# Optimization experiments

Hardware: AMD Instinct MI355X
Metric: run time of the kernel (lower is better)

## Reference

```python
import jax, jax.numpy as jnp
import numpy as np
import math

B, S, D, H, WIDTH, NHW = 8, 1024, 512, 8, 8, 2
DK = D // H
S2 = S + 2 * WIDTH


def setup_inputs() -> dict:
    key = jax.random.key(0)
    ks = jax.random.split(key, 12)
    sc = 1.0 / math.sqrt(D)
    return {
        "x": jax.random.normal(ks[0], (B, S, D), jnp.float32),
        "l_attn_W": jax.random.normal(ks[1], (4, D, D), jnp.float32) * sc,  # q,k,v,out
        "l_attn_b": jnp.zeros((4, D), jnp.float32),
        "r_attn_W": jax.random.normal(ks[2], (4, D, D), jnp.float32) * sc,
        "r_attn_b": jnp.zeros((4, D), jnp.float32),
        "left_pad": jax.random.normal(ks[3], (WIDTH, D), jnp.float32) * sc,
        "right_pad": jax.random.normal(ks[4], (WIDTH, D), jnp.float32) * sc,
        "left_w": jax.random.normal(ks[5], (WIDTH + 1,), jnp.float32),
        "right_w": jax.random.normal(ks[6], (WIDTH + 1,), jnp.float32),
        "l_hw_W": jax.random.normal(ks[7], (NHW, D, 2 * D), jnp.float32) * sc,
        "l_hw_b": jnp.zeros((NHW, 2 * D), jnp.float32),
        "r_hw_W": jax.random.normal(ks[8], (NHW, D, 2 * D), jnp.float32) * sc,
        "r_hw_b": jnp.zeros((NHW, 2 * D), jnp.float32),
    }


def _mha(x, W, b, mask):
    # x: [B, S2, D]; W: [4, D, D]; mask: [1, S2, S2] bool (True = keep)
    q = (x @ W[0] + b[0]).reshape(B, S2, H, DK)
    k = (x @ W[1] + b[1]).reshape(B, S2, H, DK)
    v = (x @ W[2] + b[2]).reshape(B, S2, H, DK)
    scores = jnp.einsum('bihd,bjhd->bhij', q, k) / math.sqrt(DK)
    scores = jnp.where(mask[:, None], scores, jnp.float32(-1e9))
    p = jax.nn.softmax(scores, axis=-1)
    o = jnp.einsum('bhij,bjhd->bihd', p, v).reshape(B, S2, D)
    return o @ W[3] + b[3]


def _highway(x, Ws, bs):
    # AllenNLP-style Highway: projected -> [nonlinear | gate]
    for i in range(NHW):
        proj = x @ Ws[i] + bs[i]
        nl = jax.nn.relu(proj[..., :D])
        g = jax.nn.sigmoid(proj[..., D:])
        x = g * x + (1.0 - g) * nl
    return x


def reference(x, l_attn_W, l_attn_b, r_attn_W, r_attn_b, left_pad, right_pad,
              left_w, right_w, l_hw_W, l_hw_b, r_hw_W, r_hw_b):
    new_in = jnp.concatenate([
        jnp.broadcast_to(left_pad, (B, WIDTH, D)), x,
        jnp.broadcast_to(right_pad, (B, WIDTH, D))], axis=1)  # [B, S2, D]
    idx = jnp.arange(S2)
    diff = idx[:, None] - idx[None, :]
    lmask = ((diff >= 0) & (diff <= WIDTH + 1))[None]          # attend to [i-width-1, i]
    rmask = ((diff <= 0) & (diff >= -(WIDTH + 1)))[None]       # attend to [i, i+width+1]
    nl_attn = _mha(new_in, l_attn_W, l_attn_b, lmask)
    nr_attn = _mha(new_in, r_attn_W, r_attn_b, rmask)
    left_out = nl_attn[:, WIDTH:WIDTH + S, :]   # position end = start + width
    right_out = nr_attn[:, WIDTH:WIDTH + S, :]
    # relative-position weighted sliding windows (vectorized over all steps)
    lrel = sum(left_w[j] * new_in[:, j:j + S, :] for j in range(WIDTH + 1))
    rrel = sum(right_w[j] * new_in[:, WIDTH + j:WIDTH + j + S, :] for j in range(WIDTH + 1))
    left_out = _highway(left_out + lrel, l_hw_W, l_hw_b)
    right_out = _highway(right_out + rrel, r_hw_W, r_hw_b)
    out = jnp.concatenate([left_out, right_out], axis=-1)  # [B, S, 2D]
    return out[None]  # [1, B, S, 2D] matching torch stack layout
```

## Files before the change

### kernel.cpp

```cpp
#include <hip/hip_runtime.h>


#define B_ 8
#define S_ 1024
#define D_ 512
#define H_ 8
#define DK_ 64
#define WIDTH_ 8
#define S2_ 1040
#define NHW_ 2

typedef short bf16x8 __attribute__((ext_vector_type(8)));
typedef float f32x4 __attribute__((ext_vector_type(4)));

__device__ __forceinline__ float us2f(unsigned short u) {
  union { unsigned int i; float f; } c; c.i = ((unsigned int)u) << 16; return c.f;
}
__device__ __forceinline__ unsigned short f2us(float f) {
  union { float f; unsigned int i; } c; c.f = f;
  unsigned int x = c.i;
  return (unsigned short)((x + 0x7fffu + ((x >> 16) & 1u)) >> 16);
}
__device__ __forceinline__ unsigned int pack2(float a, float b) {
  return (unsigned int)f2us(a) | ((unsigned int)f2us(b) << 16);
}
__device__ __forceinline__ void async16(const void* g, void* l) {
  __builtin_amdgcn_global_load_lds(
      (const __attribute__((address_space(1))) void*)g,
      (__attribute__((address_space(3))) void*)l, 16, 0, 0);
}
__device__ __forceinline__ void unpack8(uint4 u, float* f) {
  unsigned int w[4] = {u.x, u.y, u.z, u.w};
  #pragma unroll
  for (int c = 0; c < 4; ++c) {
    union { unsigned int i; float g; } lo, hi;
    lo.i = w[c] << 16;
    hi.i = w[c] & 0xffff0000u;
    f[2 * c] = lo.g;
    f[2 * c + 1] = hi.g;
  }
}

__global__ __launch_bounds__(256) void k_prep(
    const float* __restrict__ x,
    const float* __restrict__ lpad, const float* __restrict__ rpad,
    const float* __restrict__ lW, const float* __restrict__ rW,
    const float* __restrict__ lb, const float* __restrict__ rb,
    const float* __restrict__ lhwW, const float* __restrict__ rhwW,
    unsigned short* __restrict__ WTall, unsigned short* __restrict__ WTp,
    unsigned short* __restrict__ hWT,
    unsigned short* __restrict__ nin, float* __restrict__ qkvbias)
{
  __shared__ float tile[32][33];
  const size_t DD = (size_t)D_ * D_;
  int bx = blockIdx.x;
  int tx = threadIdx.x & 31, ty = threadIdx.x >> 5;

  if (bx < 2048) {
    int sl = bx >> 8, rem = bx & 255;
    int side = sl >> 2, slice = sl & 3;
    int c0 = (rem & 15) * 32, r0 = (rem >> 4) * 32;
    const float* src = (side ? rW : lW) + (size_t)slice * DD;
    unsigned short* dst = (slice < 3) ? WTall + (size_t)(side * 3 + slice) * DD
                                      : WTp + (size_t)side * DD;
    #pragma unroll
    for (int i = 0; i < 4; ++i)
      tile[ty + i * 8][tx] = src[(size_t)(r0 + ty + i * 8) * D_ + c0 + tx];
    __syncthreads();
    #pragma unroll
    for (int i = 0; i < 4; ++i)
      dst[(size_t)(c0 + ty + i * 8) * D_ + r0 + tx] = f2us(tile[tx][ty + i * 8]);
    return;
  }
  if (bx < 4096) {
    int idx = bx - 2048;
    int sl = idx >> 9, rem = idx & 511;
    int c0 = (rem & 31) * 32, r0 = (rem >> 5) * 32;
    const float* src = ((sl >> 1) ? rhwW : lhwW) + (size_t)(sl & 1) * 512 * 1024;
    unsigned short* dst = hWT + (size_t)sl * 1024 * 512;
    #pragma unroll
    for (int i = 0; i < 4; ++i)
      tile[ty + i * 8][tx] = src[(size_t)(r0 + ty + i * 8) * 1024 + c0 + tx];
    __syncthreads();
    #pragma unroll
    for (int i = 0; i < 4; ++i) {
      int c = c0 + ty + i * 8;
      int q = (2 * ((c & 511) >> 4) + (c >= 512 ? 1 : 0)) * 16 + (c & 15);
      dst[(size_t)q * 512 + r0 + tx] = f2us(tile[tx][ty + i * 8]);
    }
    return;
  }
  int gid = (bx - 4096) * 256 + threadIdx.x;
  const int NTH = B_ * S2_ * 64;
  if (gid >= NTH) {
    int t = gid - NTH;
    if (t < 1536) qkvbias[t] = lb[t];
    else if (t < 3072) qkvbias[t] = rb[t - 1536];
    return;
  }
  int c8 = (gid & 63) << 3;
  int row = gid >> 6;
  int b = row / S2_;
  int t = row - b * S2_;
  const float* src;
  if (t < WIDTH_)            src = lpad + (size_t)t * D_ + c8;
  else if (t >= S_ + WIDTH_) src = rpad + (size_t)(t - S_ - WIDTH_) * D_ + c8;
  else                       src = x + ((size_t)b * S_ + (t - WIDTH_)) * D_ + c8;
  float4 a = *reinterpret_cast<const float4*>(src);
  float4 c = *reinterpret_cast<const float4*>(src + 4);
  uint4 o;
  o.x = pack2(a.x, a.y); o.y = pack2(a.z, a.w);
  o.z = pack2(c.x, c.y); o.w = pack2(c.z, c.w);
  *reinterpret_cast<uint4*>(nin + (size_t)row * D_ + c8) = o;
}

__global__ __launch_bounds__(256) void k_gemm_mfma(
    const unsigned short* __restrict__ A,
    const unsigned short* __restrict__ BT,
    const float* __restrict__ bias,
    unsigned short* __restrict__ C,
    int M, int N, int K)
{
  __shared__ unsigned short As[128 * 64];
  __shared__ unsigned short Bs[128 * 64];

  const int tid = threadIdx.x;
  const int w = tid >> 6;
  const int l = tid & 63;
  const int bm = blockIdx.y * 128;
  const int bn = blockIdx.x * 128;
  const int wrow = (w >> 1) * 64;
  const int wcol = (w & 1) * 64;

  const int lr = l >> 3;
  const int sk = (((l & 7) ^ lr) & 7) * 8;
  const unsigned short* Ap = A + (size_t)(bm + w * 8 + lr) * K + sk;
  const unsigned short* Bp = BT + (size_t)(bn + w * 8 + lr) * K + sk;
  unsigned short* lA = &As[w * 512];
  unsigned short* lB = &Bs[w * 512];
  const size_t K32 = (size_t)32 * K;

  const int fl = l & 15;
  const int fq = l >> 4;
  const int fx = fl & 7;

  f32x4 acc[4][4];
  #pragma unroll
  for (int mi = 0; mi < 4; ++mi)
    #pragma unroll
    for (int ni = 0; ni < 4; ++ni) acc[mi][ni] = (f32x4){0.f, 0.f, 0.f, 0.f};

  for (int k0 = 0; k0 < K; k0 += 64) {
    #pragma unroll
    for (int r = 0; r < 4; ++r) {
      async16(Ap + k0 + r * K32, lA + r * 2048);
      async16(Bp + k0 + r * K32, lB + r * 2048);
    }
    __syncthreads();
    #pragma unroll
    for (int s = 0; s < 2; ++s) {
      bf16x8 af[4], bfr[4];
      #pragma unroll
      for (int mi = 0; mi < 4; ++mi)
        af[mi] = *reinterpret_cast<const bf16x8*>(
            &As[(wrow + mi * 16 + fl) * 64 + (((s * 4 + fq) ^ fx) * 8)]);
      #pragma unroll
      for (int ni = 0; ni < 4; ++ni)
        bfr[ni] = *reinterpret_cast<const bf16x8*>(
            &Bs[(wcol + ni * 16 + fl) * 64 + (((s * 4 + fq) ^ fx) * 8)]);
      #pragma unroll
      for (int mi = 0; mi < 4; ++mi)
        #pragma unroll
        for (int ni = 0; ni < 4; ++ni)
          acc[mi][ni] = __builtin_amdgcn_mfma_f32_16x16x32_bf16(
              af[mi], bfr[ni], acc[mi][ni], 0, 0, 0);
    }
    __syncthreads();
  }

  float bv[4];
  #pragma unroll
  for (int ni = 0; ni < 4; ++ni) bv[ni] = bias[bn + wcol + ni * 16 + fl];

  const int rbase = (l >> 4) * 4;
  #pragma unroll
  for (int mi = 0; mi < 4; ++mi) {
    #pragma unroll
    for (int r = 0; r < 4; ++r) {
      int row = bm + wrow + mi * 16 + rbase + r;
      unsigned short* Cp = C + (size_t)row * N + bn + wcol + fl;
      #pragma unroll
      for (int ni = 0; ni < 4; ++ni)
        Cp[ni * 16] = f2us(acc[mi][ni][r] + bv[ni]);
    }
  }
}

__global__ __launch_bounds__(256) void k_gemm_proj(
    const unsigned short* __restrict__ ctx,
    const unsigned short* __restrict__ WTp,
    const unsigned short* __restrict__ nin,
    const float* __restrict__ lb3, const float* __restrict__ rb3,
    const float* __restrict__ wrel0, const float* __restrict__ wrel1,
    unsigned short* __restrict__ hwx)
{
  __shared__ unsigned short smem[128 * 136];
  unsigned short* As = smem;
  unsigned short* Bs = smem + 8192;
  const int K = 512, N = 512;
  const size_t MS = (size_t)B_ * S_ * D_;

  const int z = blockIdx.z;
  const unsigned short* A = ctx + (size_t)z * MS;
  const unsigned short* BT = WTp + (size_t)z * 512 * 512;
  const float* bias = z ? rb3 : lb3;
  const float* wrel = z ? wrel1 : wrel0;
  const int off = z * WIDTH_;

  const int tid = threadIdx.x;
  const int w = tid >> 6;
  const int l = tid & 63;
  const int bm = blockIdx.y * 128;
  const int bn = blockIdx.x * 128;
  const int wrow = (w >> 1) * 64;
  const int wcol = (w & 1) * 64;

  const int lr = l >> 3;
  const int sk = (((l & 7) ^ lr) & 7) * 8;
  const unsigned short* Ap = A + (size_t)(bm + w * 8 + lr) * K + sk;
  const unsigned short* Bp = BT + (size_t)(bn + w * 8 + lr) * K + sk;
  unsigned short* lA = &As[w * 512];
  unsigned short* lB = &Bs[w * 512];
  const size_t K32 = (size_t)32 * K;

  const int fl = l & 15;
  const int fq = l >> 4;
  const int fx = fl & 7;

  f32x4 acc[4][4];
  #pragma unroll
  for (int mi = 0; mi < 4; ++mi)
    #pragma unroll
    for (int ni = 0; ni < 4; ++ni) acc[mi][ni] = (f32x4){0.f, 0.f, 0.f, 0.f};

  for (int k0 = 0; k0 < K; k0 += 64) {
    #pragma unroll
    for (int r = 0; r < 4; ++r) {
      async16(Ap + k0 + r * K32, lA + r * 2048);
      async16(Bp + k0 + r * K32, lB + r * 2048);
    }
    __syncthreads();
    #pragma unroll
    for (int s = 0; s < 2; ++s) {
      bf16x8 af[4], bfr[4];
      #pragma unroll
      for (int mi = 0; mi < 4; ++mi)
        af[mi] = *reinterpret_cast<const bf16x8*>(
            &As[(wrow + mi * 16 + fl) * 64 + (((s * 4 + fq) ^ fx) * 8)]);
      #pragma unroll
      for (int ni = 0; ni < 4; ++ni)
        bfr[ni] = *reinterpret_cast<const bf16x8*>(
            &Bs[(wcol + ni * 16 + fl) * 64 + (((s * 4 + fq) ^ fx) * 8)]);
      #pragma unroll
      for (int mi = 0; mi < 4; ++mi)
        #pragma unroll
        for (int ni = 0; ni < 4; ++ni)
          acc[mi][ni] = __builtin_amdgcn_mfma_f32_16x16x32_bf16(
              af[mi], bfr[ni], acc[mi][ni], 0, 0, 0);
    }
    __syncthreads();
  }

  float bv[4];
  #pragma unroll
  for (int ni = 0; ni < 4; ++ni) bv[ni] = bias[bn + wcol + ni * 16 + fl];
  const int rbase = (l >> 4) * 4;
  #pragma unroll
  for (int mi = 0; mi < 4; ++mi)
    #pragma unroll
    for (int r = 0; r < 4; ++r)
      #pragma unroll
      for (int ni = 0; ni < 4; ++ni)
        smem[(wrow + mi * 16 + rbase + r) * 136 + wcol + ni * 16 + fl] =
            f2us(acc[mi][ni][r] + bv[ni]);
  __syncthreads();

  const int trow = tid >> 4;
  const int tcol = (tid & 15) * 8;
  const float w0 = wrel[0], w1 = wrel[1], w2 = wrel[2], w3 = wrel[3],
              w4 = wrel[4], w5 = wrel[5], w6 = wrel[6], w7 = wrel[7],
              w8 = wrel[8];
  const float wj[9] = {w0, w1, w2, w3, w4, w5, w6, w7, w8};
  #pragma unroll
  for (int i = 0; i < 8; ++i) {
    int r = trow + i * 16;
    int gr = bm + r;
    int b = gr >> 10, s = gr & (S_ - 1);
    float a8[8];
    unpack8(*reinterpret_cast<const uint4*>(&smem[r * 136 + tcol]), a8);
    const unsigned short* np =
        nin + ((size_t)b * S2_ + off + s) * D_ + bn + tcol;
    #pragma unroll
    for (int j = 0; j < 9; ++j) {
      float nf[8];
      unpack8(*reinterpret_cast<const uint4*>(np + (size_t)j * D_), nf);
      #pragma unroll
      for (int e = 0; e < 8; ++e) a8[e] += wj[j] * nf[e];
    }
    uint4 o;
    o.x = pack2(a8[0], a8[1]); o.y = pack2(a8[2], a8[3]);
    o.z = pack2(a8[4], a8[5]); o.w = pack2(a8[6], a8[7]);
    *reinterpret_cast<uint4*>(
        hwx + (size_t)z * MS + (size_t)gr * D_ + bn + tcol) = o;
  }
}

template <bool FINAL>
__global__ __launch_bounds__(256) void k_gemm_hw(
    const unsigned short* __restrict__ Xsrc,
    const unsigned short* __restrict__ BT, size_t bStrZ,
    const float* __restrict__ bias0, const float* __restrict__ bias1,
    unsigned short* __restrict__ Obf,
    float* __restrict__ Ofp)
{
  __shared__ unsigned short As[128 * 64];
  __shared__ unsigned short Bs[128 * 64];
  const int K = 512;
  const size_t MS = (size_t)B_ * S_ * D_;

  const int z = blockIdx.z;
  const unsigned short* A = Xsrc + (size_t)z * MS;
  BT += (size_t)z * bStrZ;
  const float* bias = z ? bias1 : bias0;

  const int tid = threadIdx.x;
  const int w = tid >> 6;
  const int l = tid & 63;
  const int bm = blockIdx.y * 128;
  const int bn = blockIdx.x * 128;
  const int wrow = (w >> 1) * 64;
  const int wcol = (w & 1) * 64;

  const int lr = l >> 3;
  const int sk = (((l & 7) ^ lr) & 7) * 8;
  const unsigned short* Ap = A + (size_t)(bm + w * 8 + lr) * K + sk;
  const unsigned short* Bp = BT + (size_t)(bn + w * 8 + lr) * K + sk;
  unsigned short* lA = &As[w * 512];
  unsigned short* lB = &Bs[w * 512];
  const size_t K32 = (size_t)32 * K;

  const int fl = l & 15;
  const int fq = l >> 4;
  const int fx = fl & 7;

  f32x4 acc[4][4];
  #pragma unroll
  for (int mi = 0; mi < 4; ++mi)
    #pragma unroll
    for (int ni = 0; ni < 4; ++ni) acc[mi][ni] = (f32x4){0.f, 0.f, 0.f, 0.f};

  for (int k0 = 0; k0 < K; k0 += 64) {
    #pragma unroll
    for (int r = 0; r < 4; ++r) {
      async16(Ap + k0 + r * K32, lA + r * 2048);
      async16(Bp + k0 + r * K32, lB + r * 2048);
    }
    __syncthreads();
    #pragma unroll
    for (int s = 0; s < 2; ++s) {
      bf16x8 af[4], bfr[4];
      #pragma unroll
      for (int mi = 0; mi < 4; ++mi)
        af[mi] = *reinterpret_cast<const bf16x8*>(
            &As[(wrow + mi * 16 + fl) * 64 + (((s * 4 + fq) ^ fx) * 8)]);
      #pragma unroll
      for (int ni = 0; ni < 4; ++ni)
        bfr[ni] = *reinterpret_cast<const bf16x8*>(
            &Bs[(wcol + ni * 16 + fl) * 64 + (((s * 4 + fq) ^ fx) * 8)]);
      #pragma unroll
      for (int mi = 0; mi < 4; ++mi)
        #pragma unroll
        for (int ni = 0; ni < 4; ++ni)
          acc[mi][ni] = __builtin_amdgcn_mfma_f32_16x16x32_bf16(
              af[mi], bfr[ni], acc[mi][ni], 0, 0, 0);
    }
    __syncthreads();
  }

  const int ocb = ((bn + wcol) >> 1) + fl;
  float bnl[2], bg[2];
  #pragma unroll
  for (int p = 0; p < 2; ++p) {
    bnl[p] = bias[ocb + p * 16];
    bg[p]  = bias[512 + ocb + p * 16];
  }

  const int rbase = (l >> 4) * 4;
  #pragma unroll
  for (int mi = 0; mi < 4; ++mi) {
    #pragma unroll
    for (int r = 0; r < 4; ++r) {
      int row = bm + wrow + mi * 16 + rbase + r;
      #pragma unroll
      for (int p = 0; p < 2; ++p) {
        int oc = ocb + p * 16;
        float nl = fmaxf(acc[mi][2 * p][r] + bnl[p], 0.f);
        float g  = 1.f / (1.f + __expf(-(acc[mi][2 * p + 1][r] + bg[p])));
        float xv = us2f(A[(size_t)row * 512 + oc]);
        float res = g * xv + (1.f - g) * nl;
        if (FINAL) Ofp[(size_t)row * 1024 + z * 512 + oc] = res;
        else       Obf[(size_t)z * MS + (size_t)row * 512 + oc] = f2us(res);
      }
    }
  }
}

__global__ __launch_bounds__(256) void k_attn_window(
    const unsigned short* __restrict__ qkv,
    unsigned short* __restrict__ ctx)
{
  int wid = (blockIdx.x * 256 + threadIdx.x) >> 6;
  int lane = threadIdx.x & 63;
  int s = wid & (S_ - 1);
  int b = (wid >> 10) & (B_ - 1);
  int dir = wid >> 13;
  int i = s + WIDTH_;

  const size_t base = (size_t)b * S2_ * 3072 + dir * 1536;
  const int c0 = lane * 8;

  float qf[8];
  unpack8(*reinterpret_cast<const uint4*>(qkv + base + (size_t)i * 3072 + c0), qf);

  float sc[10];
  float mx = -1e30f;
  #pragma unroll
  for (int t = 0; t < 10; ++t) {
    int j = (dir == 0) ? (i - 9 + t) : (i + t);
    float sv = -1e30f;
    if (j >= 0 && j < S2_) {
      float kf[8];
      unpack8(*reinterpret_cast<const uint4*>(
          qkv + base + (size_t)j * 3072 + 512 + c0), kf);
      float p = qf[0] * kf[0];
      #pragma unroll
      for (int e = 1; e < 8; ++e) p += qf[e] * kf[e];
      p += __shfl_xor(p, 1);
      p += __shfl_xor(p, 2);
      p += __shfl_xor(p, 4);
      sv = p * 0.125f;
    }
    sc[t] = sv;
    mx = fmaxf(mx, sv);
  }

  float denom = 0.f;
  #pragma unroll
  for (int t = 0; t < 10; ++t) {
    sc[t] = (sc[t] > -1e29f) ? __expf(sc[t] - mx) : 0.f;
    denom += sc[t];
  }
  float inv = 1.f / denom;

  float acc[8] = {0.f, 0.f, 0.f, 0.f, 0.f, 0.f, 0.f, 0.f};
  #pragma unroll
  for (int t = 0; t < 10; ++t) {
    int j = (dir == 0) ? (i - 9 + t) : (i + t);
    if (j >= 0 && j < S2_) {
      float vf[8];
      unpack8(*reinterpret_cast<const uint4*>(
          qkv + base + (size_t)j * 3072 + 1024 + c0), vf);
      float p = sc[t];
      #pragma unroll
      for (int e = 0; e < 8; ++e) acc[e] += p * vf[e];
    }
  }

  uint4 o;
  o.x = pack2(acc[0] * inv, acc[1] * inv);
  o.y = pack2(acc[2] * inv, acc[3] * inv);
  o.z = pack2(acc[4] * inv, acc[5] * inv);
  o.w = pack2(acc[6] * inv, acc[7] * inv);
  *reinterpret_cast<uint4*>(
      ctx + (((size_t)dir * B_ + b) * S_ + s) * D_ + c0) = o;
}

extern "C" void kernel_launch(void* const* d_in, const int* in_sizes, int n_in,
                              void* d_out, int out_size, void* d_ws, size_t ws_size,
                              hipStream_t stream) {
  const float* x    = (const float*)d_in[0];
  const float* lW   = (const float*)d_in[1];
  const float* lb   = (const float*)d_in[2];
  const float* rW   = (const float*)d_in[3];
  const float* rb   = (const float*)d_in[4];
  const float* lpad = (const float*)d_in[5];
  const float* rpad = (const float*)d_in[6];
  const float* lw   = (const float*)d_in[7];
  const float* rw   = (const float*)d_in[8];
  const float* lhwW = (const float*)d_in[9];
  const float* lhwb = (const float*)d_in[10];
  const float* rhwW = (const float*)d_in[11];
  const float* rhwb = (const float*)d_in[12];
  float* out = (float*)d_out;
  unsigned short* ws = (unsigned short*)d_ws;

  const size_t NIN  = (size_t)B_ * S2_ * D_;
  const size_t NQKV = (size_t)B_ * S2_ * 3072;
  const size_t MS   = (size_t)B_ * S_ * D_;
  const size_t DD   = (size_t)D_ * D_;
  const size_t LHW  = (size_t)1024 * 512;

  unsigned short* nin   = ws;
  unsigned short* qkv   = nin + NIN;
  unsigned short* ctx   = qkv + NQKV;
  unsigned short* hwx   = ctx + 2 * MS;
  unsigned short* hwy   = hwx + 2 * MS;
  unsigned short* WTall = hwy + 2 * MS;
  unsigned short* WTp   = WTall + 6 * DD;
  unsigned short* hWT   = WTp + 2 * DD;
  float* qkvbias        = (float*)(hWT + 4 * LHW);

  k_prep<<<6188, 256, 0, stream>>>(x, lpad, rpad, lW, rW, lb, rb, lhwW, rhwW,
                                   WTall, WTp, hWT, nin, qkvbias);

  const int MQ = B_ * S2_;

  {
    dim3 g(3072 / 128, MQ / 128, 1);
    k_gemm_mfma<<<g, 256, 0, stream>>>(nin, WTall, qkvbias, qkv, MQ, 3072, D_);
  }

  k_attn_window<<<(2 * B_ * S_) / 4, 256, 0, stream>>>(qkv, ctx);

  {
    dim3 g(D_ / 128, (B_ * S_) / 128, 2);
    k_gemm_proj<<<g, 256, 0, stream>>>(ctx, WTp, nin, lb + 3 * D_, rb + 3 * D_,
                                       lw, rw, hwx);
  }

  {
    dim3 g(1024 / 128, (B_ * S_) / 128, 2);
    k_gemm_hw<false><<<g, 256, 0, stream>>>(hwx, hWT, 2 * LHW,
                                            lhwb, rhwb, hwy, nullptr);
    k_gemm_hw<true><<<g, 256, 0, stream>>>(hwy, hWT + LHW, 2 * LHW,
                                           lhwb + 1024, rhwb + 1024,
                                           nullptr, out);
  }
}
```

Baseline: 249.1 us.

## Replace 128x128 GEMMs with double-buffered 256x256 eight-wave MFMA kernel

Replaces the QKV and highway GEMM kernels with a single templated 256x256-tile kernel that uses 512 threads, 128KB of shared memory, and a double-buffered async-load pipeline. Each K-tile is split into quadrants so global loads overlap with MFMA work, and MFMA sections run at raised wave priority. The highway weight column permutation is changed to match the new tile layout, and M rows are clamped for the non-multiple QKV M dimension. Larger tiles raise arithmetic intensity and cut global traffic, at the cost of fewer blocks (lower occupancy and wave-quantisation risk) and a tightly hand-ordered barrier schedule.

```diff
diff --git a/kernel.cpp b/kernel.cpp
--- a/kernel.cpp
+++ b/kernel.cpp
@@ -85,7 +85,11 @@
     #pragma unroll
     for (int i = 0; i < 4; ++i) {
       int c = c0 + ty + i * 8;
-      int q = (2 * ((c & 511) >> 4) + (c >= 512 ? 1 : 0)) * 16 + (c & 15);
+      int cm = c & 511;
+      int j = cm >> 4;
+      int jl = j & 7;
+      int Bq = ((jl >> 2) << 3) + (jl & 3) + ((c >= 512) ? 4 : 0);
+      int q = (j >> 3) * 256 + Bq * 16 + (cm & 15);
       dst[(size_t)q * 512 + r0 + tx] = f2us(tile[tx][ty + i * 8]);
     }
     return;
@@ -114,84 +118,163 @@
   *reinterpret_cast<uint4*>(nin + (size_t)row * D_ + c8) = o;
 }
 
-__global__ __launch_bounds__(256) void k_gemm_mfma(
-    const unsigned short* __restrict__ A,
-    const unsigned short* __restrict__ BT,
-    const float* __restrict__ bias,
-    unsigned short* __restrict__ C,
-    int M, int N, int K)
+template <int EPI>
+__global__ __launch_bounds__(512, 2) void k_gemm256(
+    const unsigned short* __restrict__ Abase, size_t aStrZ,
+    const unsigned short* __restrict__ BTbase, size_t bStrZ,
+    const float* __restrict__ bias0, const float* __restrict__ bias1,
+    unsigned short* __restrict__ Cbf, float* __restrict__ Cfp,
+    int M, int N)
 {
-  __shared__ unsigned short As[128 * 64];
-  __shared__ unsigned short Bs[128 * 64];
-
+  __shared__ __align__(16) unsigned short smem[65536];
   const int tid = threadIdx.x;
-  const int w = tid >> 6;
-  const int l = tid & 63;
-  const int bm = blockIdx.y * 128;
-  const int bn = blockIdx.x * 128;
-  const int wrow = (w >> 1) * 64;
-  const int wcol = (w & 1) * 64;
-
-  const int lr = l >> 3;
-  const int sk = (((l & 7) ^ lr) & 7) * 8;
-  const unsigned short* Ap = A + (size_t)(bm + w * 8 + lr) * K + sk;
-  const unsigned short* Bp = BT + (size_t)(bn + w * 8 + lr) * K + sk;
-  unsigned short* lA = &As[w * 512];
-  unsigned short* lB = &Bs[w * 512];
-  const size_t K32 = (size_t)32 * K;
-
-  const int fl = l & 15;
-  const int fq = l >> 4;
-  const int fx = fl & 7;
-
-  f32x4 acc[4][4];
-  #pragma unroll
-  for (int mi = 0; mi < 4; ++mi)
+  const int w = tid >> 6, l = tid & 63;
+  const int wm = w >> 2, wn = w & 3;
+  const int fl = l & 15, fq = l >> 4;
+  const int z = blockIdx.z;
+  const unsigned short* A = Abase + (size_t)z * aStrZ;
+  const unsigned short* BT = BTbase + (size_t)z * bStrZ;
+  const int bm = blockIdx.y * 256, bn = blockIdx.x * 256;
+
+  const int xorv = ((fl >> 2) & 1) << 5;
+  const int cs0 = ((fq * 16) ^ xorv) >> 1;
+  const int cs1 = ((64 + fq * 16) ^ xorv) >> 1;
+
+  const int loff = (l * 16) ^ ((l >= 32) ? 32 : 0);
+  const int rr = loff >> 7;
+  const int ce = (loff & 127) >> 1;
+  const unsigned short* gA[2][2];
+  const unsigned short* gB[2][2];
+  #pragma unroll
+  for (int i = 0; i < 2; ++i)
+    #pragma unroll
+    for (int h = 0; h < 2; ++h) {
+      int ra = bm + h * 128 + (2 * w + i) * 8 + rr;
+      if (ra > M - 1) ra = M - 1;
+      gA[i][h] = A + (size_t)ra * 512 + ce;
+      int rb = bn + h * 128 + (2 * w + i) * 8 + rr;
+      gB[i][h] = BT + (size_t)rb * 512 + ce;
+    }
+
+  f32x4 acc[8][4];
+  #pragma unroll
+  for (int mi = 0; mi < 8; ++mi)
     #pragma unroll
     for (int ni = 0; ni < 4; ++ni) acc[mi][ni] = (f32x4){0.f, 0.f, 0.f, 0.f};
 
-  for (int k0 = 0; k0 < K; k0 += 64) {
-    #pragma unroll
-    for (int r = 0; r < 4; ++r) {
-      async16(Ap + k0 + r * K32, lA + r * 2048);
-      async16(Bp + k0 + r * K32, lB + r * 2048);
-    }
-    __syncthreads();
-    #pragma unroll
-    for (int s = 0; s < 2; ++s) {
-      bf16x8 af[4], bfr[4];
-      #pragma unroll
-      for (int mi = 0; mi < 4; ++mi)
-        af[mi] = *reinterpret_cast<const bf16x8*>(
-            &As[(wrow + mi * 16 + fl) * 64 + (((s * 4 + fq) ^ fx) * 8)]);
-      #pragma unroll
-      for (int ni = 0; ni < 4; ++ni)
-        bfr[ni] = *reinterpret_cast<const bf16x8*>(
-            &Bs[(wcol + ni * 16 + fl) * 64 + (((s * 4 + fq) ^ fx) * 8)]);
-      #pragma unroll
-      for (int mi = 0; mi < 4; ++mi)
+  bf16x8 ar[4][2], br[2][2];
+
+#define BAR() __builtin_amdgcn_s_barrier()
+#define STGA(buf, h, kt) do { \
+    async16(gA[0][h] + (kt) * 64, &smem[((buf) * 2 + (h)) * 8192 + (2 * w) * 512]); \
+    async16(gA[1][h] + (kt) * 64, &smem[((buf) * 2 + (h)) * 8192 + (2 * w + 1) * 512]); } while (0)
+#define STGB(buf, h, kt) do { \
+    async16(gB[0][h] + (kt) * 64, &smem[32768 + ((buf) * 2 + (h)) * 8192 + (2 * w) * 512]); \
+    async16(gB[1][h] + (kt) * 64, &smem[32768 + ((buf) * 2 + (h)) * 8192 + (2 * w + 1) * 512]); } while (0)
+#define LDA(buf, h) do { const unsigned short* p_ = &smem[((buf) * 2 + (h)) * 8192]; \
+    _Pragma("unroll") for (int m4 = 0; m4 < 4; ++m4) { \
+      int ro_ = ((2 * m4 + wm) * 16 + fl) * 64; \
+      ar[m4][0] = *reinterpret_cast<const bf16x8*>(p_ + ro_ + cs0); \
+      ar[m4][1] = *reinterpret_cast<const bf16x8*>(p_ + ro_ + cs1); } } while (0)
+#define LDB(buf, h) do { const unsigned short* p_ = &smem[32768 + ((buf) * 2 + (h)) * 8192]; \
+    _Pragma("unroll") for (int n2 = 0; n2 < 2; ++n2) { \
+      int ro_ = ((4 * n2 + wn) * 16 + fl) * 64; \
+      br[n2][0] = *reinterpret_cast<const bf16x8*>(p_ + ro_ + cs0); \
+      br[n2][1] = *reinterpret_cast<const bf16x8*>(p_ + ro_ + cs1); } } while (0)
+#define QUAD(miH, niH) do { __builtin_amdgcn_s_setprio(1); \
+    _Pragma("unroll") for (int m4 = 0; m4 < 4; ++m4) \
+      _Pragma("unroll") for (int n2 = 0; n2 < 2; ++n2) \
+        _Pragma("unroll") for (int s_ = 0; s_ < 2; ++s_) \
+          acc[(miH) * 4 + m4][(niH) * 2 + n2] = __builtin_amdgcn_mfma_f32_16x16x32_bf16( \
+              ar[m4][s_], br[n2][s_], acc[(miH) * 4 + m4][(niH) * 2 + n2], 0, 0, 0); \
+    __builtin_amdgcn_s_setprio(0); } while (0)
+
+  STGA(0, 0, 0); STGB(0, 0, 0); STGB(0, 1, 0); STGA(0, 1, 0);
+  STGA(1, 0, 1); STGB(1, 1, 1); STGA(1, 1, 1);
+  asm volatile("s_waitcnt vmcnt(6)" ::: "memory");
+  BAR();
+
+  #pragma unroll 1
+  for (int it = 0; it < 4; ++it) {
+    const int t1 = 2 * it + 1, t2 = 2 * it + 2, t3 = 2 * it + 3;
+    LDA(0, 0); LDB(0, 0);
+    STGB(1, 0, t1);
+    BAR(); QUAD(0, 0); BAR();
+    LDB(0, 1);
+    if (t2 < 8) STGA(0, 0, t2);
+    BAR(); QUAD(0, 1); BAR();
+    LDA(0, 1);
+    if (t2 < 8) STGB(0, 1, t2);
+    BAR(); QUAD(1, 1); BAR();
+    LDB(0, 0);
+    if (t2 < 8) STGA(0, 1, t2);
+    BAR(); QUAD(1, 0);
+    if (it < 3) asm volatile("s_waitcnt vmcnt(6)" ::: "memory");
+    else        asm volatile("s_waitcnt vmcnt(0)" ::: "memory");
+    BAR();
+    LDA(1, 0); LDB(1, 0);
+    if (t2 < 8) STGB(0, 0, t2);
+    BAR(); QUAD(0, 0); BAR();
+    LDB(1, 1);
+    if (t3 < 8) STGA(1, 0, t3);
+    BAR(); QUAD(0, 1); BAR();
+    LDA(1, 1);
+    if (t3 < 8) STGB(1, 1, t3);
+    BAR(); QUAD(1, 1); BAR();
+    LDB(1, 0);
+    if (t3 < 8) STGA(1, 1, t3);
+    BAR(); QUAD(1, 0);
+    asm volatile("s_waitcnt vmcnt(6)" ::: "memory");
+    BAR();
+  }
+#undef BAR
+#undef STGA
+#undef STGB
+#undef LDA
+#undef LDB
+#undef QUAD
+
+  if (EPI == 0) {
+    float bv[4];
+    #pragma unroll
+    for (int ni = 0; ni < 4; ++ni) bv[ni] = bias0[bn + (4 * ni + wn) * 16 + fl];
+    #pragma unroll
+    for (int mi = 0; mi < 8; ++mi) {
+      #pragma unroll
+      for (int r = 0; r < 4; ++r) {
+        int gr = bm + (2 * mi + wm) * 16 + fq * 4 + r;
+        if (gr < M) {
+          unsigned short* Cp = Cbf + (size_t)gr * N + bn + wn * 16 + fl;
+          #pragma unroll
+          for (int ni = 0; ni < 4; ++ni) Cp[ni * 64] = f2us(acc[mi][ni][r] + bv[ni]);
+        }
+      }
+    }
+  } else {
+    const float* bias = z ? bias1 : bias0;
+    const size_t MS = (size_t)B_ * S_ * D_;
+    float bnl[2], bg[2]; int xs[2];
+    #pragma unroll
+    for (int np = 0; np < 2; ++np) {
+      xs[np] = (blockIdx.x * 8 + np * 4 + wn) * 16 + fl;
+      bnl[np] = bias[xs[np]];
+      bg[np]  = bias[512 + xs[np]];
+    }
+    #pragma unroll
+    for (int mi = 0; mi < 8; ++mi) {
+      #pragma unroll
+      for (int r = 0; r < 4; ++r) {
+        int gr = bm + (2 * mi + wm) * 16 + fq * 4 + r;
         #pragma unroll
-        for (int ni = 0; ni < 4; ++ni)
-          acc[mi][ni] = __builtin_amdgcn_mfma_f32_16x16x32_bf16(
-              af[mi], bfr[ni], acc[mi][ni], 0, 0, 0);
-    }
-    __syncthreads();
-  }
-
-  float bv[4];
-  #pragma unroll
-  for (int ni = 0; ni < 4; ++ni) bv[ni] = bias[bn + wcol + ni * 16 + fl];
-
-  const int rbase = (l >> 4) * 4;
-  #pragma unroll
-  for (int mi = 0; mi < 4; ++mi) {
-    #pragma unroll
-    for (int r = 0; r < 4; ++r) {
-      int row = bm + wrow + mi * 16 + rbase + r;
-      unsigned short* Cp = C + (size_t)row * N + bn + wcol + fl;
-      #pragma unroll
-      for (int ni = 0; ni < 4; ++ni)
-        Cp[ni * 16] = f2us(acc[mi][ni][r] + bv[ni]);
+        for (int np = 0; np < 2; ++np) {
+          float nl = fmaxf(acc[mi][2 * np][r] + bnl[np], 0.f);
+          float g  = 1.f / (1.f + __expf(-(acc[mi][2 * np + 1][r] + bg[np])));
+          float xv = us2f(A[(size_t)gr * 512 + xs[np]]);
+          float res = g * xv + (1.f - g) * nl;
+          if (EPI == 2) Cfp[(size_t)gr * 1024 + (size_t)z * 512 + xs[np]] = res;
+          else Cbf[(size_t)z * MS + (size_t)gr * 512 + xs[np]] = f2us(res);
+        }
+      }
     }
   }
 }
@@ -312,106 +395,6 @@
     o.z = pack2(a8[4], a8[5]); o.w = pack2(a8[6], a8[7]);
     *reinterpret_cast<uint4*>(
         hwx + (size_t)z * MS + (size_t)gr * D_ + bn + tcol) = o;
-  }
-}
-
-template <bool FINAL>
-__global__ __launch_bounds__(256) void k_gemm_hw(
-    const unsigned short* __restrict__ Xsrc,
-    const unsigned short* __restrict__ BT, size_t bStrZ,
-    const float* __restrict__ bias0, const float* __restrict__ bias1,
-    unsigned short* __restrict__ Obf,
-    float* __restrict__ Ofp)
-{
-  __shared__ unsigned short As[128 * 64];
-  __shared__ unsigned short Bs[128 * 64];
-  const int K = 512;
-  const size_t MS = (size_t)B_ * S_ * D_;
-
-  const int z = blockIdx.z;
-  const unsigned short* A = Xsrc + (size_t)z * MS;
-  BT += (size_t)z * bStrZ;
-  const float* bias = z ? bias1 : bias0;
-
-  const int tid = threadIdx.x;
-  const int w = tid >> 6;
-  const int l = tid & 63;
-  const int bm = blockIdx.y * 128;
-  const int bn = blockIdx.x * 128;
-  const int wrow = (w >> 1) * 64;
-  const int wcol = (w & 1) * 64;
-
-  const int lr = l >> 3;
-  const int sk = (((l & 7) ^ lr) & 7) * 8;
-  const unsigned short* Ap = A + (size_t)(bm + w * 8 + lr) * K + sk;
-  const unsigned short* Bp = BT + (size_t)(bn + w * 8 + lr) * K + sk;
-  unsigned short* lA = &As[w * 512];
-  unsigned short* lB = &Bs[w * 512];
-  const size_t K32 = (size_t)32 * K;
-
-  const int fl = l & 15;
-  const int fq = l >> 4;
-  const int fx = fl & 7;
-
-  f32x4 acc[4][4];
-  #pragma unroll
-  for (int mi = 0; mi < 4; ++mi)
-    #pragma unroll
-    for (int ni = 0; ni < 4; ++ni) acc[mi][ni] = (f32x4){0.f, 0.f, 0.f, 0.f};
-
-  for (int k0 = 0; k0 < K; k0 += 64) {
-    #pragma unroll
-    for (int r = 0; r < 4; ++r) {
-      async16(Ap + k0 + r * K32, lA + r * 2048);
-      async16(Bp + k0 + r * K32, lB + r * 2048);
-    }
-    __syncthreads();
-    #pragma unroll
-    for (int s = 0; s < 2; ++s) {
-      bf16x8 af[4], bfr[4];
-      #pragma unroll
-      for (int mi = 0; mi < 4; ++mi)
-        af[mi] = *reinterpret_cast<const bf16x8*>(
-            &As[(wrow + mi * 16 + fl) * 64 + (((s * 4 + fq) ^ fx) * 8)]);
-      #pragma unroll
-      for (int ni = 0; ni < 4; ++ni)
-        bfr[ni] = *reinterpret_cast<const bf16x8*>(
-            &Bs[(wcol + ni * 16 + fl) * 64 + (((s * 4 + fq) ^ fx) * 8)]);
-      #pragma unroll
-      for (int mi = 0; mi < 4; ++mi)
-        #pragma unroll
-        for (int ni = 0; ni < 4; ++ni)
-          acc[mi][ni] = __builtin_amdgcn_mfma_f32_16x16x32_bf16(
-              af[mi], bfr[ni], acc[mi][ni], 0, 0, 0);
-    }
-    __syncthreads();
-  }
-
-  const int ocb = ((bn + wcol) >> 1) + fl;
-  float bnl[2], bg[2];
-  #pragma unroll
-  for (int p = 0; p < 2; ++p) {
-    bnl[p] = bias[ocb + p * 16];
-    bg[p]  = bias[512 + ocb + p * 16];
-  }
-
-  const int rbase = (l >> 4) * 4;
-  #pragma unroll
-  for (int mi = 0; mi < 4; ++mi) {
-    #pragma unroll
-    for (int r = 0; r < 4; ++r) {
-      int row = bm + wrow + mi * 16 + rbase + r;
-      #pragma unroll
-      for (int p = 0; p < 2; ++p) {
-        int oc = ocb + p * 16;
-        float nl = fmaxf(acc[mi][2 * p][r] + bnl[p], 0.f);
-        float g  = 1.f / (1.f + __expf(-(acc[mi][2 * p + 1][r] + bg[p])));
-        float xv = us2f(A[(size_t)row * 512 + oc]);
-        float res = g * xv + (1.f - g) * nl;
-        if (FINAL) Ofp[(size_t)row * 1024 + z * 512 + oc] = res;
-        else       Obf[(size_t)z * MS + (size_t)row * 512 + oc] = f2us(res);
-      }
-    }
   }
 }
 
@@ -526,8 +509,9 @@
   const int MQ = B_ * S2_;
 
   {
-    dim3 g(3072 / 128, MQ / 128, 1);
-    k_gemm_mfma<<<g, 256, 0, stream>>>(nin, WTall, qkvbias, qkv, MQ, 3072, D_);
+    dim3 g(3072 / 256, 33, 1);
+    k_gemm256<0><<<g, 512, 0, stream>>>(nin, 0, WTall, 0, qkvbias, nullptr,
+                                        qkv, nullptr, MQ, 3072);
   }
 
   k_attn_window<<<(2 * B_ * S_) / 4, 256, 0, stream>>>(qkv, ctx);
@@ -539,11 +523,12 @@
   }
 
   {
-    dim3 g(1024 / 128, (B_ * S_) / 128, 2);
-    k_gemm_hw<false><<<g, 256, 0, stream>>>(hwx, hWT, 2 * LHW,
-                                            lhwb, rhwb, hwy, nullptr);
-    k_gemm_hw<true><<<g, 256, 0, stream>>>(hwy, hWT + LHW, 2 * LHW,
-                                           lhwb + 1024, rhwb + 1024,
-                                           nullptr, out);
-  }
-}
+    dim3 g(1024 / 256, (B_ * S_) / 256, 2);
+    k_gemm256<1><<<g, 512, 0, stream>>>(hwx, MS, hWT, 2 * LHW,
+                                        lhwb, rhwb, hwy, nullptr,
+                                        B_ * S_, 1024);
+    k_gemm256<2><<<g, 512, 0, stream>>>(hwy, MS, hWT + LHW, 2 * LHW,
+                                        lhwb + 1024, rhwb + 1024,
+                                        nullptr, out, B_ * S_, 1024);
+  }
+}
```

After: 243.1 us. -2.4%, faster.
